# Kernel optimization log

Hardware: AMD Instinct MI355X
Metric: run time of the kernel (lower is better)

Reference implementation:

```python
import jax, jax.numpy as jnp
import numpy as np

H, KV, D, EPS = 32, 8, 128, 1e-6
G = H // KV  # kv groups = 4
ROPE_THETA = 5000000.0


def _rms_norm(x, gamma):
    # x: (..., D)
    return x * jax.lax.rsqrt(jnp.mean(x * x, axis=-1, keepdims=True) + EPS) * gamma


def _rotate_half(x):
    x1, x2 = jnp.split(x, 2, axis=-1)
    return jnp.concatenate([-x2, x1], axis=-1)


def _apply_rope(x, cos, sin):
    # x: (b, h, s, D); cos/sin: (b, s, 1, D) -> (b, 1, s, D)
    cos = jnp.transpose(cos, (0, 2, 1, 3))
    sin = jnp.transpose(sin, (0, 2, 1, 3))
    return x * cos + _rotate_half(x) * sin


def setup_inputs() -> dict:
    key = jax.random.key(0)
    ks = jax.random.split(key, 8)
    b, s, hid = 2, 2048, 2560
    hidden = jax.random.normal(ks[0], (b, s, hid), dtype=jnp.float32)
    # realistic RoPE tables (half-split convention matching _rotate_half)
    inv_freq = 1.0 / (ROPE_THETA ** (np.arange(0, D, 2, dtype=np.float32) / D))  # (D/2,)
    pos = np.arange(s, dtype=np.float32)
    freqs = np.outer(pos, inv_freq)                     # (s, D/2)
    emb = np.concatenate([freqs, freqs], axis=-1)       # (s, D)
    cos = jnp.broadcast_to(jnp.asarray(np.cos(emb))[None, :, None, :], (b, s, 1, D))
    sin = jnp.broadcast_to(jnp.asarray(np.sin(emb))[None, :, None, :], (b, s, 1, D))
    sc = 1.0 / np.sqrt(hid)
    wq = jax.random.normal(ks[1], (H * D, hid), dtype=jnp.float32) * sc
    wk = jax.random.normal(ks[2], (KV * D, hid), dtype=jnp.float32) * sc
    wv = jax.random.normal(ks[3], (KV * D, hid), dtype=jnp.float32) * sc
    wo = jax.random.normal(ks[4], (hid, H * D), dtype=jnp.float32) * (1.0 / np.sqrt(H * D))
    q_gamma = jnp.ones((D,), dtype=jnp.float32)
    k_gamma = jnp.ones((D,), dtype=jnp.float32)
    return {"hidden": hidden, "cos": cos, "sin": sin, "wq": wq, "wk": wk,
            "wv": wv, "wo": wo, "q_gamma": q_gamma, "k_gamma": k_gamma}


def reference(hidden, cos, sin, wq, wk, wv, wo, q_gamma, k_gamma):
    b, s, _ = hidden.shape
    # projections -> (b, heads, s, D)
    q = (hidden @ wq.T).reshape(b, s, H, D).transpose(0, 2, 1, 3)
    k = (hidden @ wk.T).reshape(b, s, KV, D).transpose(0, 2, 1, 3)
    v = (hidden @ wv.T).reshape(b, s, KV, D).transpose(0, 2, 1, 3)
    # QK-RMSNorm over head_dim
    q = _rms_norm(q, q_gamma)
    k = _rms_norm(k, k_gamma)
    # RoPE
    q = _apply_rope(q, cos, sin)
    k = _apply_rope(k, cos, sin)
    new_k, new_v = k, v  # kv cache (no prior cache)
    # GQA attention without materializing expanded K/V
    qg = q.reshape(b, KV, G, s, D)
    scale = 1.0 / np.sqrt(D)
    scores = jnp.einsum('bkgqd,bkld->bkgql', qg, k) * scale  # (b,KV,G,s,s)
    causal = jnp.tril(jnp.ones((s, s), dtype=bool))
    scores = jnp.where(causal, scores, jnp.finfo(scores.dtype).min)
    probs = jax.nn.softmax(scores, axis=-1)
    out = jnp.einsum('bkgql,bkld->bkgqd', probs, v)          # (b,KV,G,s,D)
    out = out.reshape(b, H, s, D).transpose(0, 2, 1, 3).reshape(b, s, H * D)
    return (out @ wo.T, new_k, new_v)
```

## Files before the change

kernel.cpp:

```cpp
#include <hip/hip_runtime.h>
#include <stdint.h>

typedef unsigned short u16;
typedef __attribute__((ext_vector_type(8))) short short8;
typedef __attribute__((ext_vector_type(4))) float f32x4;

#define MFMA_BF16(a,b,c) __builtin_amdgcn_mfma_f32_16x16x32_bf16((a),(b),(c),0,0,0)

__device__ __forceinline__ u16 f2bf(float x) {
    uint32_t u = __builtin_bit_cast(uint32_t, x);
    u += 0x7fffu + ((u >> 16) & 1u);
    return (u16)(u >> 16);
}
__device__ __forceinline__ float bf2f(u16 u) {
    return __builtin_bit_cast(float, (uint32_t)u << 16);
}
__device__ __forceinline__ void glds16(const void* g, void* lds) {
    __builtin_amdgcn_global_load_lds((const __attribute__((address_space(1))) void*)g,
                                     (__attribute__((address_space(3))) void*)lds,
                                     16, 0, 0);
}

__global__ __launch_bounds__(256) void cvt_kernel(const float* __restrict__ src,
                                                  u16* __restrict__ dst, int n) {
    int i = (blockIdx.x * 256 + threadIdx.x) * 4;
    if (i + 4 <= n) {
        float4 v = *(const float4*)(src + i);
        ushort4 o;
        o.x = f2bf(v.x); o.y = f2bf(v.y); o.z = f2bf(v.z); o.w = f2bf(v.w);
        *(ushort4*)(dst + i) = o;
    }
}

template<bool BF16_OUT>
__global__ __launch_bounds__(256) void gemm_bt(const u16* __restrict__ A,
                                               const u16* __restrict__ B,
                                               void* __restrict__ Cv,
                                               int K, int lda, int ldb, int ldc)
{
    __shared__ __align__(16) u16 As[128 * 32];
    __shared__ __align__(16) u16 Bs[128 * 32];
    const int t = threadIdx.x;
    const int w = t >> 6, l = t & 63;
    const int m0 = blockIdx.y * 128, n0 = blockIdx.x * 128;
    const int wm = (w & 1) * 64, wn = (w >> 1) * 64;
    const int lrow = l & 15, lk = l >> 4;

    f32x4 acc[4][4];
#pragma unroll
    for (int i = 0; i < 4; i++)
#pragma unroll
        for (int j = 0; j < 4; j++) acc[i][j] = (f32x4){0.f, 0.f, 0.f, 0.f};

    const int c0 = t, c1 = t + 256;
    const int r0 = c0 >> 2, g0 = (c0 & 3) ^ ((r0 >> 1) & 3);
    const int r1 = c1 >> 2, g1 = (c1 & 3) ^ ((r1 >> 1) & 3);
    const u16* Ap0 = A + (size_t)(m0 + r0) * lda + g0 * 8;
    const u16* Ap1 = A + (size_t)(m0 + r1) * lda + g1 * 8;
    const u16* Bp0 = B + (size_t)(n0 + r0) * ldb + g0 * 8;
    const u16* Bp1 = B + (size_t)(n0 + r1) * ldb + g1 * 8;
    char* Asb = (char*)As + w * 1024;
    char* Bsb = (char*)Bs + w * 1024;

    for (int k0 = 0; k0 < K; k0 += 32) {
        __syncthreads();
        glds16(Ap0 + k0, Asb);
        glds16(Ap1 + k0, Asb + 4096);
        glds16(Bp0 + k0, Bsb);
        glds16(Bp1 + k0, Bsb + 4096);
        __syncthreads();
        short8 af[4], bf[4];
#pragma unroll
        for (int mi = 0; mi < 4; mi++) {
            int r = wm + mi * 16 + lrow;
            int sl = lk ^ ((r >> 1) & 3);
            af[mi] = *(const short8*)&As[r * 32 + sl * 8];
        }
#pragma unroll
        for (int ni = 0; ni < 4; ni++) {
            int r = wn + ni * 16 + lrow;
            int sl = lk ^ ((r >> 1) & 3);
            bf[ni] = *(const short8*)&Bs[r * 32 + sl * 8];
        }
#pragma unroll
        for (int mi = 0; mi < 4; mi++)
#pragma unroll
            for (int ni = 0; ni < 4; ni++)
                acc[mi][ni] = MFMA_BF16(af[mi], bf[ni], acc[mi][ni]);
    }

#pragma unroll
    for (int mi = 0; mi < 4; mi++) {
#pragma unroll
        for (int r = 0; r < 4; r++) {
            int row = m0 + wm + mi * 16 + lk * 4 + r;
#pragma unroll
            for (int ni = 0; ni < 4; ni++) {
                int col = n0 + wn + ni * 16 + lrow;
                float v = acc[mi][ni][r];
                if (BF16_OUT) ((u16*)Cv)[(size_t)row * ldc + col] = f2bf(v);
                else          ((float*)Cv)[(size_t)row * ldc + col] = v;
            }
        }
    }
}

__global__ __launch_bounds__(256) void norm_rope_qk(const u16* __restrict__ qkv,
        const float* __restrict__ cosb, const float* __restrict__ sinb,
        const float* __restrict__ qg, const float* __restrict__ kg,
        u16* __restrict__ qb, u16* __restrict__ kb, float* __restrict__ k_out)
{
    const int idx = blockIdx.x * 4 + (threadIdx.x >> 6);
    const int l = threadIdx.x & 63;
    const int tok = idx / 40, hd = idx - tok * 40;
    const int b = tok >> 11, pos = tok & 2047;
    const u16* row = qkv + (size_t)tok * 6144 + hd * 128;
    float x1 = bf2f(row[l]), x2 = bf2f(row[l + 64]);
    float ss = x1 * x1 + x2 * x2;
#pragma unroll
    for (int m = 1; m < 64; m <<= 1) ss += __shfl_xor(ss, m, 64);
    float rn = rsqrtf(ss * (1.0f / 128.0f) + 1e-6f);

    const float* gm = (hd < 32) ? qg : kg;
    float xn1 = x1 * rn * gm[l];
    float xn2 = x2 * rn * gm[l + 64];
    float c1 = cosb[(size_t)tok * 128 + l],      s1 = sinb[(size_t)tok * 128 + l];
    float c2 = cosb[(size_t)tok * 128 + l + 64], s2 = sinb[(size_t)tok * 128 + l + 64];
    float y1 = xn1 * c1 - xn2 * s1;
    float y2 = xn2 * c2 + xn1 * s2;
    if (hd < 32) {
        const float qs = 0.08838834764831845f;
        size_t base = (((size_t)b * 32 + hd) * 2048 + pos) * 128;
        qb[base + l]      = f2bf(y1 * qs);
        qb[base + l + 64] = f2bf(y2 * qs);
    } else {
        int kv = hd - 32;
        size_t base = (((size_t)b * 8 + kv) * 2048 + pos) * 128;
        k_out[base + l] = y1; k_out[base + l + 64] = y2;
        kb[base + l] = f2bf(y1); kb[base + l + 64] = f2bf(y2);
    }
}

__global__ __launch_bounds__(256) void v_pack(const u16* __restrict__ qkv,
        float* __restrict__ v_out, u16* __restrict__ vtb)
{
    __shared__ __align__(16) u16 T[64 * 128];
    const int pb = blockIdx.x, bkv = blockIdx.y;
    const int b = bkv >> 3, kv = bkv & 7;
    const int p0 = pb * 64;
    const int t = threadIdx.x;
    const int pos = t >> 2, ch4 = t & 3;
    const u16* src = qkv + (size_t)(b * 2048 + p0 + pos) * 6144 + (40 + kv) * 128 + ch4 * 32;
    float* vdst = v_out + ((size_t)bkv * 2048 + p0 + pos) * 128 + ch4 * 32;
#pragma unroll
    for (int j = 0; j < 4; j++) {
        short8 x = *(const short8*)(src + j * 8);
        float4 f0, f1;
        f0.x = bf2f(x[0]); f0.y = bf2f(x[1]); f0.z = bf2f(x[2]); f0.w = bf2f(x[3]);
        f1.x = bf2f(x[4]); f1.y = bf2f(x[5]); f1.z = bf2f(x[6]); f1.w = bf2f(x[7]);
        *(float4*)(vdst + j * 8)     = f0;
        *(float4*)(vdst + j * 8 + 4) = f1;
        int slot = (ch4 * 4 + j) ^ (pos & 7);
        *(short8*)&T[pos * 128 + slot * 8] = x;
    }
    __syncthreads();
    const int d = t & 127, ph = t >> 7;
    u16* obase = vtb + ((size_t)bkv * 128 + d) * 2048 + p0 + ph * 32;
#pragma unroll
    for (int g = 0; g < 4; g++) {
        short8 tv;
#pragma unroll
        for (int jj = 0; jj < 8; jj++) {
            int pp = ph * 32 + g * 8 + jj;
            int slot = (d >> 3) ^ (pp & 7);
            tv[jj] = (short)T[pp * 128 + slot * 8 + (d & 7)];
        }
        *(short8*)(obase + g * 8) = tv;
    }
}

__global__ __launch_bounds__(256, 3) void attn_kernel(const u16* __restrict__ qb,
        const u16* __restrict__ kb, const u16* __restrict__ vtb,
        u16* __restrict__ ao)
{
    __shared__ __align__(16) u16 Ks[64 * 128];
    __shared__ __align__(16) u16 Vs[128 * 64];
    __shared__ __align__(16) u16 Ps[4][32 * 72];

    const int bh = blockIdx.x;
    const int b = bh >> 5, h = bh & 31;
    const int kvh = h >> 2;
    const int qt = (int)gridDim.y - 1 - (int)blockIdx.y;
    const int q0 = qt * 128;
    const int t = threadIdx.x, w = t >> 6, l = t & 63;
    const int lrow = l & 15, lk = l >> 4;

    const u16* qbase  = qb  + ((size_t)b * 32 + h)  * 2048 * 128;
    const u16* kbase  = kb  + ((size_t)b * 8 + kvh) * 2048 * 128;
    const u16* vtbase = vtb + ((size_t)b * 8 + kvh) * 128 * 2048;

    short8 qf[2][4];
#pragma unroll
    for (int m = 0; m < 2; m++) {
        const u16* qrow = qbase + (size_t)(q0 + w * 32 + m * 16 + lrow) * 128 + lk * 8;
#pragma unroll
        for (int ks = 0; ks < 4; ks++) qf[m][ks] = *(const short8*)(qrow + ks * 32);
    }

    f32x4 o[2][8];
#pragma unroll
    for (int m = 0; m < 2; m++)
#pragma unroll
        for (int i = 0; i < 8; i++) o[m][i] = (f32x4){0.f, 0.f, 0.f, 0.f};
    float lsum[2][4] = {{0.f,0.f,0.f,0.f},{0.f,0.f,0.f,0.f}};

    int kR[4], kG[4], vR[4], vG[4];
#pragma unroll
    for (int i = 0; i < 4; i++) {
        int c = i * 256 + t;
        kR[i] = c >> 4; kG[i] = (c & 15) ^ (kR[i] & 7);
        vR[i] = c >> 3; vG[i] = (c & 7)  ^ (vR[i] & 7);
    }
    char* Ksb = (char*)Ks + w * 1024;
    char* Vsb = (char*)Vs + w * 1024;
    u16* pw = &Ps[w][0];
    const int wrow_max = q0 + w * 32 + 31;

    const int nkt = 2 * qt + 2;
    for (int kt = 0; kt < nkt; kt++) {
        const int kv0 = kt * 64;
        __syncthreads();
#pragma unroll
        for (int i = 0; i < 4; i++)
            glds16(kbase + (size_t)(kv0 + kR[i]) * 128 + kG[i] * 8, Ksb + i * 4096);
#pragma unroll
        for (int i = 0; i < 4; i++)
            glds16(vtbase + (size_t)vR[i] * 2048 + kv0 + vG[i] * 8, Vsb + i * 4096);
        __syncthreads();

        if (kv0 > wrow_max) continue;

        f32x4 s[2][4];
#pragma unroll
        for (int m = 0; m < 2; m++)
#pragma unroll
            for (int i = 0; i < 4; i++) s[m][i] = (f32x4){0.f, 0.f, 0.f, 0.f};
#pragma unroll
        for (int ks = 0; ks < 4; ks++) {
#pragma unroll
            for (int nt = 0; nt < 4; nt++) {
                int r = nt * 16 + lrow;
                int sl = (ks * 4 + lk) ^ (r & 7);
                short8 kf = *(const short8*)&Ks[r * 128 + sl * 8];
                s[0][nt] = MFMA_BF16(qf[0][ks], kf, s[0][nt]);
                s[1][nt] = MFMA_BF16(qf[1][ks], kf, s[1][nt]);
            }
        }

#pragma unroll
        for (int m = 0; m < 2; m++) {
            const int rowbase = q0 + w * 32 + m * 16;
            if (kv0 + 63 > rowbase) {
#pragma unroll
                for (int nt = 0; nt < 4; nt++) {
                    int cg = kv0 + nt * 16 + lrow;
#pragma unroll
                    for (int r = 0; r < 4; r++)
                        if (cg > rowbase + lk * 4 + r) s[m][nt][r] = -1e30f;
                }
            }
#pragma unroll
            for (int nt = 0; nt < 4; nt++)
#pragma unroll
                for (int r = 0; r < 4; r++) {
                    float p = __expf(s[m][nt][r]);
                    s[m][nt][r] = p;
                    lsum[m][r] += p;
                    pw[(m * 16 + lk * 4 + r) * 72 + nt * 16 + lrow] = f2bf(p);
                }
        }
        asm volatile("s_waitcnt lgkmcnt(0)" ::: "memory");

#pragma unroll
        for (int k2 = 0; k2 < 2; k2++) {
            short8 pf0 = *(const short8*)&pw[lrow * 72 + k2 * 32 + lk * 8];
            short8 pf1 = *(const short8*)&pw[(16 + lrow) * 72 + k2 * 32 + lk * 8];
#pragma unroll
            for (int nt = 0; nt < 8; nt++) {
                int rr = nt * 16 + lrow;
                int sl = (k2 * 4 + lk) ^ (rr & 7);
                short8 vf = *(const short8*)&Vs[rr * 64 + sl * 8];
                o[0][nt] = MFMA_BF16(pf0, vf, o[0][nt]);
                o[1][nt] = MFMA_BF16(pf1, vf, o[1][nt]);
            }
        }
    }

#pragma unroll
    for (int m = 0; m < 2; m++)
#pragma unroll
        for (int r = 0; r < 4; r++) {
            float v = lsum[m][r];
            v += __shfl_xor(v, 1, 64);
            v += __shfl_xor(v, 2, 64);
            v += __shfl_xor(v, 4, 64);
            v += __shfl_xor(v, 8, 64);
            lsum[m][r] = 1.0f / v;
        }
#pragma unroll
    for (int m = 0; m < 2; m++)
#pragma unroll
        for (int nt = 0; nt < 8; nt++)
#pragma unroll
            for (int r = 0; r < 4; r++) {
                int tok = q0 + w * 32 + m * 16 + lk * 4 + r;
                size_t off = ((size_t)b * 2048 + tok) * 4096 + h * 128 + nt * 16 + lrow;
                ao[off] = f2bf(o[m][nt][r] * lsum[m][r]);
            }
}

extern "C" void kernel_launch(void* const* d_in, const int* in_sizes, int n_in,
                              void* d_out, int out_size, void* d_ws, size_t ws_size,
                              hipStream_t stream)
{
    (void)in_sizes; (void)n_in; (void)out_size; (void)ws_size;
    const float* hidden = (const float*)d_in[0];
    const float* cosb   = (const float*)d_in[1];
    const float* sinb   = (const float*)d_in[2];
    const float* wq     = (const float*)d_in[3];
    const float* wk     = (const float*)d_in[4];
    const float* wv     = (const float*)d_in[5];
    const float* wo     = (const float*)d_in[6];
    const float* qg     = (const float*)d_in[7];
    const float* kg     = (const float*)d_in[8];

    float* out   = (float*)d_out;
    float* k_out = out + (size_t)2 * 2048 * 2560;
    float* v_out = k_out + (size_t)2 * 8 * 2048 * 128;

    u16* hid_b = (u16*)d_ws;
    u16* w_b   = hid_b + 10485760;
    u16* wo_b  = w_b   + 15728640;
    u16* q_b   = wo_b  + 10485760;
    u16* k_b   = q_b   + 16777216;
    u16* vt_b  = k_b   + 4194304;
    u16* qkv_b = vt_b  + 4194304;
    u16* ao_b  = hid_b;

    cvt_kernel<<<10240, 256, 0, stream>>>(hidden, hid_b, 10485760);
    cvt_kernel<<<10240, 256, 0, stream>>>(wq, w_b, 10485760);
    cvt_kernel<<<2560,  256, 0, stream>>>(wk, w_b + 10485760, 2621440);
    cvt_kernel<<<2560,  256, 0, stream>>>(wv, w_b + 13107200, 2621440);
    cvt_kernel<<<10240, 256, 0, stream>>>(wo, wo_b, 10485760);

    gemm_bt<true><<<dim3(48, 32), 256, 0, stream>>>(hid_b, w_b, qkv_b,
                                                    2560, 2560, 2560, 6144);
    norm_rope_qk<<<40960, 256, 0, stream>>>(qkv_b, cosb, sinb, qg, kg,
                                            q_b, k_b, k_out);
    v_pack<<<dim3(32, 16), 256, 0, stream>>>(qkv_b, v_out, vt_b);
    attn_kernel<<<dim3(64, 16), 256, 0, stream>>>(q_b, k_b, vt_b, ao_b);
    gemm_bt<false><<<dim3(20, 32), 256, 0, stream>>>(ao_b, wo_b, out,
                                                     4096, 4096, 4096, 2560);
}
```

Before: 674.9 us.

## Double GEMM K-tile to 64 with new LDS swizzle and fuse conversion launches

The bf16 GEMM now stages 64-wide K slices per iteration instead of 32, using a new XOR swizzle over 8 16-byte groups and two MFMA sub-steps per barrier pair. This halves the number of __syncthreads round trips and issues more global-to-LDS loads per wait. The cost is doubled LDS use per block, which may reduce occupancy. Separately, the five fp32-to-bf16 conversion launches are merged into one kernel that dispatches by index range, removing launch overhead.

```diff
diff --git a/kernel.cpp b/kernel.cpp
--- a/kernel.cpp
+++ b/kernel.cpp
@@ -21,15 +21,26 @@
                                      16, 0, 0);
 }
 
-__global__ __launch_bounds__(256) void cvt_kernel(const float* __restrict__ src,
-                                                  u16* __restrict__ dst, int n) {
+__device__ __forceinline__ void cvt4(const float* __restrict__ s,
+                                     u16* __restrict__ d, int i) {
+    float4 v = *(const float4*)(s + i);
+    ushort4 o;
+    o.x = f2bf(v.x); o.y = f2bf(v.y); o.z = f2bf(v.z); o.w = f2bf(v.w);
+    *(ushort4*)(d + i) = o;
+}
+__global__ __launch_bounds__(256) void cvt_all(
+        const float* __restrict__ s0, u16* __restrict__ d0,
+        const float* __restrict__ s1, u16* __restrict__ d1,
+        const float* __restrict__ s2, u16* __restrict__ d2,
+        const float* __restrict__ s3, u16* __restrict__ d3,
+        const float* __restrict__ s4, u16* __restrict__ d4)
+{
     int i = (blockIdx.x * 256 + threadIdx.x) * 4;
-    if (i + 4 <= n) {
-        float4 v = *(const float4*)(src + i);
-        ushort4 o;
-        o.x = f2bf(v.x); o.y = f2bf(v.y); o.z = f2bf(v.z); o.w = f2bf(v.w);
-        *(ushort4*)(dst + i) = o;
-    }
+    if      (i < 10485760) cvt4(s0, d0, i);
+    else if (i < 20971520) cvt4(s1, d1, i - 10485760);
+    else if (i < 23592960) cvt4(s2, d2, i - 20971520);
+    else if (i < 26214400) cvt4(s3, d3, i - 23592960);
+    else if (i < 36700160) cvt4(s4, d4, i - 26214400);
 }
 
 template<bool BF16_OUT>
@@ -38,8 +49,8 @@
                                                void* __restrict__ Cv,
                                                int K, int lda, int ldb, int ldc)
 {
-    __shared__ __align__(16) u16 As[128 * 32];
-    __shared__ __align__(16) u16 Bs[128 * 32];
+    __shared__ __align__(16) u16 As[128 * 64];
+    __shared__ __align__(16) u16 Bs[128 * 64];
     const int t = threadIdx.x;
     const int w = t >> 6, l = t & 63;
     const int m0 = blockIdx.y * 128, n0 = blockIdx.x * 128;
@@ -52,41 +63,40 @@
 #pragma unroll
         for (int j = 0; j < 4; j++) acc[i][j] = (f32x4){0.f, 0.f, 0.f, 0.f};
 
-    const int c0 = t, c1 = t + 256;
-    const int r0 = c0 >> 2, g0 = (c0 & 3) ^ ((r0 >> 1) & 3);
-    const int r1 = c1 >> 2, g1 = (c1 & 3) ^ ((r1 >> 1) & 3);
-    const u16* Ap0 = A + (size_t)(m0 + r0) * lda + g0 * 8;
-    const u16* Ap1 = A + (size_t)(m0 + r1) * lda + g1 * 8;
-    const u16* Bp0 = B + (size_t)(n0 + r0) * ldb + g0 * 8;
-    const u16* Bp1 = B + (size_t)(n0 + r1) * ldb + g1 * 8;
+    const int row_b = w * 8 + (l >> 3);
+    const int gsw = ((l & 7) ^ (l >> 3)) * 8;
+    const u16* Ap[4]; const u16* Bp[4];
+#pragma unroll
+    for (int i = 0; i < 4; i++) {
+        Ap[i] = A + (size_t)(m0 + row_b + i * 32) * lda + gsw;
+        Bp[i] = B + (size_t)(n0 + row_b + i * 32) * ldb + gsw;
+    }
     char* Asb = (char*)As + w * 1024;
     char* Bsb = (char*)Bs + w * 1024;
 
-    for (int k0 = 0; k0 < K; k0 += 32) {
+    for (int k0 = 0; k0 < K; k0 += 64) {
         __syncthreads();
-        glds16(Ap0 + k0, Asb);
-        glds16(Ap1 + k0, Asb + 4096);
-        glds16(Bp0 + k0, Bsb);
-        glds16(Bp1 + k0, Bsb + 4096);
+#pragma unroll
+        for (int i = 0; i < 4; i++) glds16(Ap[i] + k0, Asb + i * 4096);
+#pragma unroll
+        for (int i = 0; i < 4; i++) glds16(Bp[i] + k0, Bsb + i * 4096);
         __syncthreads();
-        short8 af[4], bf[4];
-#pragma unroll
-        for (int mi = 0; mi < 4; mi++) {
-            int r = wm + mi * 16 + lrow;
-            int sl = lk ^ ((r >> 1) & 3);
-            af[mi] = *(const short8*)&As[r * 32 + sl * 8];
-        }
-#pragma unroll
-        for (int ni = 0; ni < 4; ni++) {
-            int r = wn + ni * 16 + lrow;
-            int sl = lk ^ ((r >> 1) & 3);
-            bf[ni] = *(const short8*)&Bs[r * 32 + sl * 8];
-        }
-#pragma unroll
-        for (int mi = 0; mi < 4; mi++)
+#pragma unroll
+        for (int k2 = 0; k2 < 2; k2++) {
+            const int slb = (k2 * 4 + lk) ^ (lrow & 7);
+            short8 af[4], bf[4];
+#pragma unroll
+            for (int mi = 0; mi < 4; mi++)
+                af[mi] = *(const short8*)&As[(wm + mi * 16 + lrow) * 64 + slb * 8];
 #pragma unroll
             for (int ni = 0; ni < 4; ni++)
-                acc[mi][ni] = MFMA_BF16(af[mi], bf[ni], acc[mi][ni]);
+                bf[ni] = *(const short8*)&Bs[(wn + ni * 16 + lrow) * 64 + slb * 8];
+#pragma unroll
+            for (int mi = 0; mi < 4; mi++)
+#pragma unroll
+                for (int ni = 0; ni < 4; ni++)
+                    acc[mi][ni] = MFMA_BF16(af[mi], bf[ni], acc[mi][ni]);
+        }
     }
 
 #pragma unroll
@@ -347,11 +357,9 @@
     u16* qkv_b = vt_b  + 4194304;
     u16* ao_b  = hid_b;
 
-    cvt_kernel<<<10240, 256, 0, stream>>>(hidden, hid_b, 10485760);
-    cvt_kernel<<<10240, 256, 0, stream>>>(wq, w_b, 10485760);
-    cvt_kernel<<<2560,  256, 0, stream>>>(wk, w_b + 10485760, 2621440);
-    cvt_kernel<<<2560,  256, 0, stream>>>(wv, w_b + 13107200, 2621440);
-    cvt_kernel<<<10240, 256, 0, stream>>>(wo, wo_b, 10485760);
+    cvt_all<<<35840, 256, 0, stream>>>(hidden, hid_b, wq, w_b,
+                                       wk, w_b + 10485760, wv, w_b + 13107200,
+                                       wo, wo_b);
 
     gemm_bt<true><<<dim3(48, 32), 256, 0, stream>>>(hid_b, w_b, qkv_b,
                                                     2560, 2560, 2560, 6144);
```

Result: no change. 661.8 us (-1.9%).
